# Performance work log

Measured on AMD Instinct MI355X. Metric: run time of the kernel, lower is better.

The kernel has to match this reference:

```python
import jax, jax.numpy as jnp
import numpy as np

MODEL_SIZE = 512
HEADS = 8
T = 2048
B = 2


def setup_inputs() -> dict:
    key = jax.random.key(0)
    ks = jax.random.split(key, 10)
    E = MODEL_SIZE
    w = 0.02  # weight init scale for numerical stability
    return {
        "input": jax.random.normal(ks[0], (T, B, E), jnp.float32),
        "pos": jax.random.normal(ks[1], (T, 1, E), jnp.float32),
        "in_proj_weight": jax.random.normal(ks[2], (3 * E, E), jnp.float32) * w,
        "out_proj_weight": jax.random.normal(ks[3], (E, E), jnp.float32) * w,
        "pos_proj_weight": jax.random.normal(ks[4], (E, E), jnp.float32) * w,
        "in_proj_bias": jax.random.normal(ks[5], (3 * E,), jnp.float32) * w,
        "out_proj_bias": jax.random.normal(ks[6], (E,), jnp.float32) * w,
        "pos_proj_bias": jax.random.normal(ks[7], (E,), jnp.float32) * w,
        "r_w_bias": jax.random.normal(ks[8], (HEADS, E // HEADS), jnp.float32) * w,
        "r_r_bias": jax.random.normal(ks[9], (HEADS, E // HEADS), jnp.float32) * w,
    }


def _rel_shift(x):
    # x: [B, H, T, R] -> Transformer-XL relative shift
    b, h, t, r = x.shape
    x = jnp.pad(x, ((0, 0), (0, 0), (0, 0), (1, 0)))  # [B,H,T,R+1]
    x = x.reshape(b, h, r + 1, t)[:, :, 1:, :]        # drop first row
    return x.reshape(b, h, t, r)


def reference(input, pos, in_proj_weight, out_proj_weight, pos_proj_weight,
              in_proj_bias, out_proj_bias, pos_proj_bias, r_w_bias, r_r_bias):
    t, b, e = input.shape
    h = r_w_bias.shape[0]
    d = e // h
    scale = 1.0 / np.sqrt(d).astype(np.float32)

    # fused QKV projection (time-first layout [T,B,E])
    qkv = input @ in_proj_weight.T + in_proj_bias          # [T,B,3E]
    q, k, v = jnp.split(qkv, 3, axis=-1)
    q = q.reshape(t, b, h, d)
    k = k.reshape(t, b, h, d)
    v = v.reshape(t, b, h, d)

    # relative position projection (pos batch dim is 1)
    r = (pos[:, 0] @ pos_proj_weight.T + pos_proj_bias).reshape(-1, h, d)  # [R,H,D]

    # content (AC) and position (BD) scores
    ac = jnp.einsum('tbhd,sbhd->bhts', q + r_w_bias, k)    # [B,H,T,T]
    bd = jnp.einsum('tbhd,rhd->bhtr', q + r_r_bias, r)     # [B,H,T,R]
    bd = _rel_shift(bd)[..., :t]

    attn = jax.nn.softmax((ac + bd) * scale, axis=-1)      # [B,H,T,T]
    ctx = jnp.einsum('bhts,sbhd->tbhd', attn, v).reshape(t, b, e)
    return ctx @ out_proj_weight.T + out_proj_bias
```

## Files before the change

kernel.cpp:

```cpp
#include <hip/hip_runtime.h>

#define T_SEQ 2048
#define BATCH 2
#define HEADS 8
#define DHEAD 64
#define EMB   512

typedef __attribute__((ext_vector_type(8))) short short8;
typedef __attribute__((ext_vector_type(4))) float floatx4;
typedef __attribute__((ext_vector_type(8))) unsigned short ushort8;
typedef __attribute__((ext_vector_type(4))) unsigned short ushort4v;

__device__ __forceinline__ unsigned short f2b(float f) {
    union { float f; unsigned u; } v; v.f = f;
    unsigned r = v.u + 0x7fffu + ((v.u >> 16) & 1u);
    return (unsigned short)(r >> 16);
}
__device__ __forceinline__ unsigned short f2bt(float f) {
    union { float f; unsigned u; } v; v.f = f;
    return (unsigned short)(v.u >> 16);
}
__device__ __forceinline__ float b2f(unsigned short s) {
    union { unsigned u; float f; } v; v.u = ((unsigned)s) << 16; return v.f;
}
__device__ __forceinline__ short8 ld_frag(const unsigned short* p) {
    ushort4v lo = *(const ushort4v*)p;
    ushort4v hi = *(const ushort4v*)(p + 4);
    short8 r;
    r[0] = lo[0]; r[1] = lo[1]; r[2] = lo[2]; r[3] = lo[3];
    r[4] = hi[0]; r[5] = hi[1]; r[6] = hi[2]; r[7] = hi[3];
    return r;
}
__device__ __forceinline__ void st8(unsigned short* p, ushort8 v) {
    ushort4v lo = { v[0], v[1], v[2], v[3] };
    ushort4v hi = { v[4], v[5], v[6], v[7] };
    *(ushort4v*)p = lo;
    *(ushort4v*)(p + 4) = hi;
}
__device__ __forceinline__ void gl16(const unsigned short* g, unsigned short* l) {
    __builtin_amdgcn_global_load_lds(
        (const __attribute__((address_space(1))) unsigned int*)g,
        (__attribute__((address_space(3))) unsigned int*)l, 16, 0, 0);
}
#define MFMA16(a, b, c) __builtin_amdgcn_mfma_f32_16x16x32_bf16(a, b, c, 0, 0, 0)

__global__ __launch_bounds__(256)
void cvt_all(const float* __restrict__ s0, const float* __restrict__ s1,
             const float* __restrict__ s2, const float* __restrict__ s3,
             const float* __restrict__ s4,
             unsigned short* __restrict__ d0, unsigned short* __restrict__ d1,
             unsigned short* __restrict__ d2, unsigned short* __restrict__ d3,
             unsigned short* __restrict__ d4)
{
    const int i = blockIdx.x * 256 + threadIdx.x;
    const float* s; unsigned short* d; int off;
    if      (i <  524288) { s = s0; d = d0; off = i; }
    else if (i <  786432) { s = s1; d = d1; off = i -  524288; }
    else if (i <  983040) { s = s2; d = d2; off = i -  786432; }
    else if (i < 1048576) { s = s3; d = d3; off = i -  983040; }
    else if (i < 1114112) { s = s4; d = d4; off = i - 1048576; }
    else return;
    const float4 v = ((const float4*)s)[off];
    ushort4v o = { f2b(v.x), f2b(v.y), f2b(v.z), f2b(v.w) };
    ((ushort4v*)d)[off] = o;
}

__global__ __launch_bounds__(256)
void gemm_qkv_pos(const unsigned short* __restrict__ inb, const unsigned short* __restrict__ w_inb,
                  const float* __restrict__ b_in,
                  const unsigned short* __restrict__ posb, const unsigned short* __restrict__ w_posb,
                  const float* __restrict__ b_pos,
                  unsigned short* __restrict__ q_s, unsigned short* __restrict__ k_s,
                  unsigned short* __restrict__ vT, unsigned short* __restrict__ r_b)
{
    __shared__ unsigned short shmem[24576];
    unsigned short* tb = shmem;

    const int id = blockIdx.x;
    const bool isPos = (id >= 768);
    const int bx = isPos ? ((id - 768) & 3) : (id % 12);
    const int by = isPos ? ((id - 768) >> 2) : (id / 12);
    const unsigned short* A = isPos ? posb : inb;
    const unsigned short* B = isPos ? w_posb : w_inb;
    const float* bias = isPos ? b_pos : b_in;

    const int bm  = by * 64;
    const int bn  = bx * 128;
    const int tid = threadIdx.x;
    const int lane = tid & 63, w = tid >> 6;
    const int m16 = lane & 15, quad = lane >> 4;
    const int wm = (w & 1) * 32, wn = (w >> 1) * 64;
    const int lrow = lane >> 3;
    const int lcol8 = lane & 7;

    floatx4 acc[2][4];
    #pragma unroll
    for (int i = 0; i < 2; ++i)
        #pragma unroll
        for (int j = 0; j < 4; ++j) acc[i][j] = (floatx4){0.f, 0.f, 0.f, 0.f};

    auto stage = [&](int q, int k0) {
        unsigned short* Ad = shmem + q * 12288;
        unsigned short* Bd = Ad + 4096;
        #pragma unroll
        for (int i = 0; i < 2; ++i) {
            const int rb  = w * 16 + i * 8;
            const int row = rb + lrow;
            const int sc  = ((lcol8 ^ (row & 7)) * 8);
            gl16(A + (size_t)(bm + row) * 512 + k0 + sc, Ad + rb * 64);
        }
        #pragma unroll
        for (int i = 0; i < 4; ++i) {
            const int rb  = w * 32 + i * 8;
            const int row = rb + lrow;
            const int sc  = ((lcol8 ^ (row & 7)) * 8);
            gl16(B + (size_t)(bn + row) * 512 + k0 + sc, Bd + rb * 64);
        }
    };
    auto frag = [&](const unsigned short* Ts, int row, int ks) {
        const int u = (ks * 4 + quad) ^ (row & 7);
        return ld_frag(&Ts[row * 64 + u * 8]);
    };

    stage(0, 0);
    __syncthreads();

    for (int kt = 0; kt < 8; ++kt) {
        const int p = kt & 1;
        unsigned short* As = shmem + p * 12288;
        unsigned short* Bs = As + 4096;
        if (kt + 1 < 8) stage(1 - p, (kt + 1) * 64);
        #pragma unroll
        for (int ks = 0; ks < 2; ++ks) {
            short8 af[2], bf[4];
            #pragma unroll
            for (int f = 0; f < 2; ++f)
                af[f] = frag(As, wm + f * 16 + m16, ks);
            #pragma unroll
            for (int f = 0; f < 4; ++f)
                bf[f] = frag(Bs, wn + f * 16 + m16, ks);
            #pragma unroll
            for (int fm = 0; fm < 2; ++fm)
                #pragma unroll
                for (int fn = 0; fn < 4; ++fn)
                    acc[fm][fn] = MFMA16(af[fm], bf[fn], acc[fm][fn]);
        }
        __syncthreads();
    }

    if (isPos) {
        #pragma unroll
        for (int fn = 0; fn < 4; ++fn) {
            const int n = bn + wn + fn * 16 + m16;
            const float bv = bias[n];
            #pragma unroll
            for (int fm = 0; fm < 2; ++fm)
                #pragma unroll
                for (int rgi = 0; rgi < 4; ++rgi) {
                    const int m = bm + wm + fm * 16 + quad * 4 + rgi;
                    r_b[(size_t)m * EMB + n] = f2b(acc[fm][fn][rgi] + bv);
                }
        }
    } else if (bn < 1024) {
        #pragma unroll
        for (int fn = 0; fn < 4; ++fn) {
            const int n = bn + wn + fn * 16 + m16;
            const float bv = bias[n];
            const int reg = n >> 9, c = n & 511, h = c >> 6, dd = c & 63;
            unsigned short* dst = reg == 0 ? q_s : k_s;
            #pragma unroll
            for (int fm = 0; fm < 2; ++fm)
                #pragma unroll
                for (int rgi = 0; rgi < 4; ++rgi) {
                    const int m = bm + wm + fm * 16 + quad * 4 + rgi;
                    const int t = m >> 1, b = m & 1;
                    dst[((size_t)(b * HEADS + h) * T_SEQ + t) * DHEAD + dd] = f2b(acc[fm][fn][rgi] + bv);
                }
        }
    } else {
        #pragma unroll
        for (int fn = 0; fn < 4; ++fn) {
            const int nl = wn + fn * 16 + m16;
            const float bv = bias[bn + nl];
            #pragma unroll
            for (int fm = 0; fm < 2; ++fm)
                #pragma unroll
                for (int rgi = 0; rgi < 4; ++rgi) {
                    const int ml = wm + fm * 16 + quad * 4 + rgi;
                    tb[nl * 67 + ml] = f2b(acc[fm][fn][rgi] + bv);
                }
        }
        __syncthreads();
        const int t0g = bm >> 1;
        for (int s2 = tid; s2 < 1024; s2 += 256) {
            const int nl = s2 >> 3;
            const int bsel = (s2 >> 2) & 1;
            const int j = s2 & 3;
            ushort8 o;
            #pragma unroll
            for (int k = 0; k < 8; ++k)
                o[k] = tb[nl * 67 + ((j * 8 + k) * 2 + bsel)];
            const int c = bn + nl - 1024, h = c >> 6, dd = c & 63;
            *(ushort8*)(vT + ((size_t)(bsel * HEADS + h) * DHEAD + dd) * T_SEQ + t0g + j * 8) = o;
        }
    }
}

__global__ __launch_bounds__(256)
void gemm_out(const unsigned short* __restrict__ A, const unsigned short* __restrict__ B,
              const float* __restrict__ bias, float* __restrict__ out)
{
    __shared__ unsigned short shmem[16384];
    const int bm  = blockIdx.y * 64;
    const int bn  = blockIdx.x * 64;
    const int tid = threadIdx.x;
    const int lane = tid & 63, w = tid >> 6;
    const int m16 = lane & 15, quad = lane >> 4;
    const int wm = (w & 1) * 32, wn = (w >> 1) * 32;
    const int lrow = lane >> 3;
    const int lcol8 = lane & 7;

    floatx4 acc[2][2];
    #pragma unroll
    for (int i = 0; i < 2; ++i)
        #pragma unroll
        for (int j = 0; j < 2; ++j) acc[i][j] = (floatx4){0.f, 0.f, 0.f, 0.f};

    auto stage = [&](int q, int k0) {
        unsigned short* Ad = shmem + q * 8192;
        unsigned short* Bd = Ad + 4096;
        #pragma unroll
        for (int i = 0; i < 2; ++i) {
            const int rb  = w * 16 + i * 8;
            const int row = rb + lrow;
            const int sc  = ((lcol8 ^ (row & 7)) * 8);
            gl16(A + (size_t)(bm + row) * 512 + k0 + sc, Ad + rb * 64);
            gl16(B + (size_t)(bn + row) * 512 + k0 + sc, Bd + rb * 64);
        }
    };
    auto frag = [&](const unsigned short* Ts, int row, int ks) {
        const int u = (ks * 4 + quad) ^ (row & 7);
        return ld_frag(&Ts[row * 64 + u * 8]);
    };

    stage(0, 0);
    __syncthreads();

    for (int kt = 0; kt < 8; ++kt) {
        const int p = kt & 1;
        unsigned short* As = shmem + p * 8192;
        unsigned short* Bs = As + 4096;
        if (kt + 1 < 8) stage(1 - p, (kt + 1) * 64);
        #pragma unroll
        for (int ks = 0; ks < 2; ++ks) {
            short8 af[2], bf[2];
            #pragma unroll
            for (int f = 0; f < 2; ++f) {
                af[f] = frag(As, wm + f * 16 + m16, ks);
                bf[f] = frag(Bs, wn + f * 16 + m16, ks);
            }
            #pragma unroll
            for (int fm = 0; fm < 2; ++fm)
                #pragma unroll
                for (int fn = 0; fn < 2; ++fn)
                    acc[fm][fn] = MFMA16(af[fm], bf[fn], acc[fm][fn]);
        }
        __syncthreads();
    }

    #pragma unroll
    for (int fn = 0; fn < 2; ++fn) {
        const int n = bn + wn + fn * 16 + m16;
        const float bv = bias[n];
        #pragma unroll
        for (int fm = 0; fm < 2; ++fm)
            #pragma unroll
            for (int rgi = 0; rgi < 4; ++rgi) {
                const int m = bm + wm + fm * 16 + quad * 4 + rgi;
                out[(size_t)m * EMB + n] = acc[fm][fn][rgi] + bv;
            }
    }
}

__global__ __launch_bounds__(256)
void attn_mfma(const unsigned short* __restrict__ qg_, const unsigned short* __restrict__ kg_,
               const unsigned short* __restrict__ vtg_, const unsigned short* __restrict__ rg_,
               const float* __restrict__ rwb, const float* __restrict__ rrb,
               unsigned short* __restrict__ ctx)
{
    const int T   = T_SEQ;
    const int tb  = blockIdx.x;
    const int t0  = tb * 64;
    const int bh  = blockIdx.y;
    const int h   = bh & 7;
    const int b   = bh >> 3;
    const int tid = threadIdx.x;
    const int lane = tid & 63;
    const int w    = tid >> 6;
    const int m16  = lane & 15;
    const int quad = lane >> 4;
    const int ibase = 16 * w + quad * 4;

    __shared__ unsigned short lds[38976];
    unsigned short* pbuf  = lds + 26112;
    unsigned short* ring  = lds + 30464;
    unsigned short* qrw_s = lds;
    unsigned short* qrr_s = lds + 8704;

    const unsigned short* qg  = qg_  + ((size_t)bh * T + t0) * DHEAD;
    const unsigned short* kg  = kg_  + (size_t)bh * T * DHEAD;
    const unsigned short* vtg = vtg_ + (size_t)bh * DHEAD * T;
    const unsigned short* rg  = rg_  + h * DHEAD;

    const float QSCALE = 0.125f * 1.44269504089f;
    for (int idx = tid; idx < 65 * 16; idx += 256) {
        const int row = idx >> 4, c = (idx & 15) << 2;
        ushort4v qv = {0, 0, 0, 0};
        if (t0 + row < T) qv = *(const ushort4v*)(qg + row * DHEAD + c);
        const float4 rr = *(const float4*)(rrb + h * DHEAD + c);
        qrr_s[row * 68 + c + 0] = f2b((b2f(qv[0]) + rr.x) * QSCALE);
        qrr_s[row * 68 + c + 1] = f2b((b2f(qv[1]) + rr.y) * QSCALE);
        qrr_s[row * 68 + c + 2] = f2b((b2f(qv[2]) + rr.z) * QSCALE);
        qrr_s[row * 68 + c + 3] = f2b((b2f(qv[3]) + rr.w) * QSCALE);
        if (row < 64) {
            const float4 rw = *(const float4*)(rwb + h * DHEAD + c);
            qrw_s[row * 68 + c + 0] = f2b((b2f(qv[0]) + rw.x) * QSCALE);
            qrw_s[row * 68 + c + 1] = f2b((b2f(qv[1]) + rw.y) * QSCALE);
            qrw_s[row * 68 + c + 2] = f2b((b2f(qv[2]) + rw.z) * QSCALE);
            qrw_s[row * 68 + c + 3] = f2b((b2f(qv[3]) + rw.w) * QSCALE);
        }
    }
    __syncthreads();

    short8 a_ac[2], a_qrl[2], a_qru[2];
    {
        const unsigned short* p0 = &qrw_s[(16 * w + m16) * 68 + quad * 8];
        a_ac[0]  = ld_frag(p0);  a_ac[1]  = ld_frag(p0 + 32);
        const unsigned short* p1 = &qrr_s[(16 * w + m16) * 68 + quad * 8];
        a_qrl[0] = ld_frag(p1);  a_qrl[1] = ld_frag(p1 + 32);
        const unsigned short* p2 = &qrr_s[(16 * w + 1 + m16) * 68 + quad * 8];
        a_qru[0] = ld_frag(p2);  a_qru[1] = ld_frag(p2 + 32);
    }

    const int srow0 = tid >> 3,          scol0 = (tid & 7) * 8;
    const int srow1 = (tid + 256) >> 3,  scol1 = (tid & 7) * 8;

    ushort8 kr[2], vr[2], rr8[2];
    auto prefetch = [&](int s0n) {
        const bool ln = (s0n <= t0);
        const int jb = (ln ? (s0n + T - t0 - 64) : (s0n - t0 - 65)) + 64;
        int j0 = jb + srow0; j0 = j0 < 0 ? 0 : (j0 > T - 1 ? T - 1 : j0);
        int j1 = jb + srow1; j1 = j1 < 0 ? 0 : (j1 > T - 1 ? T - 1 : j1);
        kr[0]  = *(const ushort8*)(kg + (size_t)(s0n + srow0) * DHEAD + scol0);
        kr[1]  = *(const ushort8*)(kg + (size_t)(s0n + srow1) * DHEAD + scol1);
        vr[0]  = *(const ushort8*)(vtg + (size_t)srow0 * T + s0n + scol0);
        vr[1]  = *(const ushort8*)(vtg + (size_t)srow1 * T + s0n + scol1);
        rr8[0] = *(const ushort8*)(rg + (size_t)j0 * EMB + scol0);
        rr8[1] = *(const ushort8*)(rg + (size_t)j1 * EMB + scol1);
    };
    auto store_bufs = [&](int q) {
        unsigned short* kb = lds + q * 4352;
        unsigned short* vb = lds + 8704 + q * 4352;
        unsigned short* rb = lds + 17408 + q * 4352;
        st8(&kb[srow0 * 68 + scol0], kr[0]);
        st8(&kb[srow1 * 68 + scol1], kr[1]);
        st8(&vb[srow0 * 68 + scol0], vr[0]);
        st8(&vb[srow1 * 68 + scol1], vr[1]);
        st8(&rb[srow0 * 68 + scol0], rr8[0]);
        st8(&rb[srow1 * 68 + scol1], rr8[1]);
    };
    auto stage_to = [&](unsigned short* dstb, int jbase) {
        #pragma unroll
        for (int idx = tid; idx < 512; idx += 256) {
            const int row = idx >> 3, c = (idx & 7) * 8;
            int j = jbase + row; j = j < 0 ? 0 : (j > T - 1 ? T - 1 : j);
            st8(&dstb[row * 68 + c], *(const ushort8*)(rg + (size_t)j * EMB + c));
        }
    };
    auto qr_half = [&](const unsigned short* rsb, const short8* aq, int slotbase) {
        #pragma unroll
        for (int cc = 0; cc < 4; ++cc) {
            floatx4 q4 = (floatx4){0.f, 0.f, 0.f, 0.f};
            #pragma unroll
            for (int ks = 0; ks < 2; ++ks) {
                short8 bfr = ld_frag(&rsb[(16 * cc + m16) * 68 + ks * 32 + quad * 8]);
                q4 = MFMA16(aq[ks], bfr, q4);
            }
            #pragma unroll
            for (int rgi = 0; rgi < 4; ++rgi)
                ring[(ibase + rgi) * 133 + slotbase + 16 * cc + m16] = f2bt(q4[rgi]);
        }
    };

    floatx4 O[4];
    float lrun[4];
    #pragma unroll
    for (int ct = 0; ct < 4; ++ct) O[ct] = (floatx4){0.f, 0.f, 0.f, 0.f};
    #pragma unroll
    for (int rgi = 0; rgi < 4; ++rgi) lrun[rgi] = 0.f;

    {
        stage_to(lds + 17408 + 4352, T - t0 - 64);
        prefetch(0);
        __syncthreads();
        qr_half(lds + 17408 + 4352, a_qrl, 0);
        store_bufs(0);
        __syncthreads();
    }

    for (int na = 0; na < T / 64; ++na) {
        const int s0 = na * 64;
        const int p = na & 1;
        unsigned short* kb = lds + p * 4352;
        unsigned short* vb = lds + 8704 + p * 4352;
        unsigned short* rp = lds + 17408 + p * 4352;
        const bool lower = (s0 <= t0);
        const int nph    = lower ? (s0 >> 6) : ((s0 - t0) >> 6);
        const int rbase  = (nph & 1) * 64;
        const int wbase  = 64 - rbase;
        const bool hasNext = (na + 1 < T / 64);

        floatx4 acf[4];
        __builtin_amdgcn_s_setprio(1);
        #pragma unroll
        for (int ct = 0; ct < 4; ++ct) {
            acf[ct] = (floatx4){0.f, 0.f, 0.f, 0.f};
            #pragma unroll
            for (int ks = 0; ks < 2; ++ks) {
                short8 bfr = ld_frag(&kb[(16 * ct + m16) * 68 + ks * 32 + quad * 8]);
                acf[ct] = MFMA16(a_ac[ks], bfr, acf[ct]);
            }
        }
        __builtin_amdgcn_s_setprio(0);
        if (hasNext) prefetch(s0 + 64);
        qr_half(rp, lower ? a_qrl : a_qru, wbase);

        if (s0 != t0) {
            #pragma unroll
            for (int ct = 0; ct < 4; ++ct) {
                #pragma unroll
                for (int rgi = 0; rgi < 4; ++rgi) {
                    const int i = ibase + rgi;
                    const int slot = ((63 - i + 16 * ct + m16) + rbase) & 127;
                    acf[ct][rgi] += b2f(ring[i * 133 + slot]);
                }
            }
            if (s0 == t0 + 64 && lane == 48 && w == 3)
                acf[0][3] -= b2f(ring[63 * 133 + (rbase & 127)]);
        } else {
            #pragma unroll
            for (int ct = 0; ct < 4; ++ct) {
                #pragma unroll
                for (int rgi = 0; rgi < 4; ++rgi) {
                    const int i = ibase + rgi, u = 16 * ct + m16;
                    if (u <= i) acf[ct][rgi] += b2f(ring[i * 133 + (((63 - i + u) + rbase) & 127)]);
                }
            }
            unsigned short* rpo = lds + 17408 + (1 - p) * 4352;
            __syncthreads();
            stage_to(rpo, -1);
            __syncthreads();
            qr_half(rpo, a_qru, 64);
            __syncthreads();
            #pragma unroll
            for (int ct = 0; ct < 4; ++ct) {
                #pragma unroll
                for (int rgi = 0; rgi < 4; ++rgi) {
                    const int i = ibase + rgi, u = 16 * ct + m16;
                    if (u >= i + 2) acf[ct][rgi] += b2f(ring[i * 133 + 63 - i + u]);
                }
            }
        }

        #pragma unroll
        for (int rgi = 0; rgi < 4; ++rgi) {
            #pragma unroll
            for (int ct = 0; ct < 4; ++ct) {
                const float pv = exp2f(acf[ct][rgi]);
                acf[ct][rgi] = pv;
                lrun[rgi] += pv;
            }
        }
        #pragma unroll
        for (int ct = 0; ct < 4; ++ct)
            #pragma unroll
            for (int rgi = 0; rgi < 4; ++rgi)
                pbuf[(ibase + rgi) * 68 + 16 * ct + m16] = f2bt(acf[ct][rgi]);

        short8 ap[2];
        {
            const unsigned short* pp = &pbuf[(16 * w + m16) * 68 + quad * 8];
            ap[0] = ld_frag(pp); ap[1] = ld_frag(pp + 32);
        }
        __builtin_amdgcn_s_setprio(1);
        #pragma unroll
        for (int ct = 0; ct < 4; ++ct) {
            #pragma unroll
            for (int ks = 0; ks < 2; ++ks) {
                short8 bfr = ld_frag(&vb[(16 * ct + m16) * 68 + ks * 32 + quad * 8]);
                O[ct] = MFMA16(ap[ks], bfr, O[ct]);
            }
        }
        __builtin_amdgcn_s_setprio(0);
        if (hasNext) store_bufs(1 - p);
        __syncthreads();
    }

    #pragma unroll
    for (int rgi = 0; rgi < 4; ++rgi) {
        float l = lrun[rgi];
        #pragma unroll
        for (int off = 1; off < 16; off <<= 1)
            l += __shfl_xor(l, off);
        const float inv = 1.f / l;
        const int t = t0 + ibase + rgi;
        #pragma unroll
        for (int ct = 0; ct < 4; ++ct)
            ctx[((size_t)t * BATCH + b) * EMB + h * DHEAD + 16 * ct + m16] = f2bt(O[ct][rgi] * inv);
    }
}

extern "C" void kernel_launch(void* const* d_in, const int* in_sizes, int n_in,
                              void* d_out, int out_size, void* d_ws, size_t ws_size,
                              hipStream_t stream)
{
    const float* input = (const float*)d_in[0];
    const float* pos   = (const float*)d_in[1];
    const float* w_in  = (const float*)d_in[2];
    const float* w_out = (const float*)d_in[3];
    const float* w_pos = (const float*)d_in[4];
    const float* b_in  = (const float*)d_in[5];
    const float* b_out = (const float*)d_in[6];
    const float* b_pos = (const float*)d_in[7];
    const float* rwb   = (const float*)d_in[8];
    const float* rrb   = (const float*)d_in[9];

    unsigned short* ws     = (unsigned short*)d_ws;
    unsigned short* inb    = ws;
    unsigned short* posb   = ws + 2097152;
    unsigned short* w_inb  = ws + 3145728;
    unsigned short* w_posb = ws + 3932160;
    unsigned short* w_outb = ws + 6291456;
    unsigned short* q_s    = ws + 6553600;
    unsigned short* k_s    = ws + 8650752;
    unsigned short* vT     = ws + 10747904;
    unsigned short* r_b    = ws + 12845056;
    unsigned short* ctx_b  = ws + 13893632;

    cvt_all<<<4352, 256, 0, stream>>>(input, pos, w_in, w_pos, w_out,
                                      inb, posb, w_inb, w_posb, w_outb);
    gemm_qkv_pos<<<896, 256, 0, stream>>>(inb, w_inb, b_in, posb, w_posb, b_pos,
                                          q_s, k_s, vT, r_b);
    attn_mfma<<<dim3(32, 16), 256, 0, stream>>>(q_s, k_s, vT, r_b, rwb, rrb, ctx_b);
    gemm_out<<<dim3(8, 64), 256, 0, stream>>>(ctx_b, w_outb, b_out, (float*)d_out);
}
```

Baseline: 183.2 us.

## Load relative-position R fragments directly from global into registers, bypassing LDS

The relative-position matrix R is no longer prefetched into a double-buffered LDS tile. Each wave now loads its MFMA B fragments for R straight from global memory into registers and feeds them to the Q·R MFMAs. This shrinks the shared-memory footprint, removes the extra staging and the three block-wide barriers on the diagonal tile, and should allow higher occupancy. The cost is per-wave global loads with less reuse and latency that is only partly hidden behind the AC MFMAs.

```diff
diff --git a/kernel.cpp b/kernel.cpp
--- a/kernel.cpp
+++ b/kernel.cpp
@@ -30,6 +30,11 @@
     r[0] = lo[0]; r[1] = lo[1]; r[2] = lo[2]; r[3] = lo[3];
     r[4] = hi[0]; r[5] = hi[1]; r[6] = hi[2]; r[7] = hi[3];
     return r;
+}
+__device__ __forceinline__ short8 ldg_frag(const unsigned short* p) {
+    union { ushort8 u; short8 s; } c;
+    c.u = *(const ushort8*)p;
+    return c.s;
 }
 __device__ __forceinline__ void st8(unsigned short* p, ushort8 v) {
     ushort4v lo = { v[0], v[1], v[2], v[3] };
@@ -301,11 +306,11 @@
     const int quad = lane >> 4;
     const int ibase = 16 * w + quad * 4;
 
-    __shared__ unsigned short lds[38976];
-    unsigned short* pbuf  = lds + 26112;
-    unsigned short* ring  = lds + 30464;
+    __shared__ unsigned short lds[30272];
+    unsigned short* pbuf  = lds + 17408;
+    unsigned short* ring  = lds + 21760;
     unsigned short* qrw_s = lds;
-    unsigned short* qrr_s = lds + 8704;
+    unsigned short* qrr_s = lds + 4352;
 
     const unsigned short* qg  = qg_  + ((size_t)bh * T + t0) * DHEAD;
     const unsigned short* kg  = kg_  + (size_t)bh * T * DHEAD;
@@ -345,47 +350,36 @@
     const int srow0 = tid >> 3,          scol0 = (tid & 7) * 8;
     const int srow1 = (tid + 256) >> 3,  scol1 = (tid & 7) * 8;
 
-    ushort8 kr[2], vr[2], rr8[2];
+    ushort8 kr[2], vr[2];
     auto prefetch = [&](int s0n) {
-        const bool ln = (s0n <= t0);
-        const int jb = (ln ? (s0n + T - t0 - 64) : (s0n - t0 - 65)) + 64;
-        int j0 = jb + srow0; j0 = j0 < 0 ? 0 : (j0 > T - 1 ? T - 1 : j0);
-        int j1 = jb + srow1; j1 = j1 < 0 ? 0 : (j1 > T - 1 ? T - 1 : j1);
         kr[0]  = *(const ushort8*)(kg + (size_t)(s0n + srow0) * DHEAD + scol0);
         kr[1]  = *(const ushort8*)(kg + (size_t)(s0n + srow1) * DHEAD + scol1);
         vr[0]  = *(const ushort8*)(vtg + (size_t)srow0 * T + s0n + scol0);
         vr[1]  = *(const ushort8*)(vtg + (size_t)srow1 * T + s0n + scol1);
-        rr8[0] = *(const ushort8*)(rg + (size_t)j0 * EMB + scol0);
-        rr8[1] = *(const ushort8*)(rg + (size_t)j1 * EMB + scol1);
     };
     auto store_bufs = [&](int q) {
         unsigned short* kb = lds + q * 4352;
         unsigned short* vb = lds + 8704 + q * 4352;
-        unsigned short* rb = lds + 17408 + q * 4352;
         st8(&kb[srow0 * 68 + scol0], kr[0]);
         st8(&kb[srow1 * 68 + scol1], kr[1]);
         st8(&vb[srow0 * 68 + scol0], vr[0]);
         st8(&vb[srow1 * 68 + scol1], vr[1]);
-        st8(&rb[srow0 * 68 + scol0], rr8[0]);
-        st8(&rb[srow1 * 68 + scol1], rr8[1]);
-    };
-    auto stage_to = [&](unsigned short* dstb, int jbase) {
-        #pragma unroll
-        for (int idx = tid; idx < 512; idx += 256) {
-            const int row = idx >> 3, c = (idx & 7) * 8;
-            int j = jbase + row; j = j < 0 ? 0 : (j > T - 1 ? T - 1 : j);
-            st8(&dstb[row * 68 + c], *(const ushort8*)(rg + (size_t)j * EMB + c));
-        }
-    };
-    auto qr_half = [&](const unsigned short* rsb, const short8* aq, int slotbase) {
+    };
+    auto ldR = [&](int jbase, short8 (&rr)[4][2]) {
+        #pragma unroll
+        for (int cc = 0; cc < 4; ++cc) {
+            int j = jbase + 16 * cc + m16; j = j < 0 ? 0 : (j > T - 1 ? T - 1 : j);
+            const unsigned short* rrow = rg + (size_t)j * EMB + quad * 8;
+            rr[cc][0] = ldg_frag(rrow);
+            rr[cc][1] = ldg_frag(rrow + 32);
+        }
+    };
+    auto qr_from = [&](short8 (&rr)[4][2], const short8* aq, int slotbase) {
         #pragma unroll
         for (int cc = 0; cc < 4; ++cc) {
             floatx4 q4 = (floatx4){0.f, 0.f, 0.f, 0.f};
-            #pragma unroll
-            for (int ks = 0; ks < 2; ++ks) {
-                short8 bfr = ld_frag(&rsb[(16 * cc + m16) * 68 + ks * 32 + quad * 8]);
-                q4 = MFMA16(aq[ks], bfr, q4);
-            }
+            q4 = MFMA16(aq[0], rr[cc][0], q4);
+            q4 = MFMA16(aq[1], rr[cc][1], q4);
             #pragma unroll
             for (int rgi = 0; rgi < 4; ++rgi)
                 ring[(ibase + rgi) * 133 + slotbase + 16 * cc + m16] = f2bt(q4[rgi]);
@@ -399,11 +393,12 @@
     #pragma unroll
     for (int rgi = 0; rgi < 4; ++rgi) lrun[rgi] = 0.f;
 
+    short8 rf[4][2];
     {
-        stage_to(lds + 17408 + 4352, T - t0 - 64);
+        ldR(T - t0 - 64, rf);
         prefetch(0);
         __syncthreads();
-        qr_half(lds + 17408 + 4352, a_qrl, 0);
+        qr_from(rf, a_qrl, 0);
         store_bufs(0);
         __syncthreads();
     }
@@ -413,12 +408,14 @@
         const int p = na & 1;
         unsigned short* kb = lds + p * 4352;
         unsigned short* vb = lds + 8704 + p * 4352;
-        unsigned short* rp = lds + 17408 + p * 4352;
         const bool lower = (s0 <= t0);
         const int nph    = lower ? (s0 >> 6) : ((s0 - t0) >> 6);
         const int rbase  = (nph & 1) * 64;
         const int wbase  = 64 - rbase;
+        const bool diag  = (s0 == t0);
         const bool hasNext = (na + 1 < T / 64);
+
+        if (!diag) ldR(lower ? (s0 + T - t0) : (s0 - t0 - 1), rf);
 
         floatx4 acf[4];
         __builtin_amdgcn_s_setprio(1);
@@ -433,9 +430,9 @@
         }
         __builtin_amdgcn_s_setprio(0);
         if (hasNext) prefetch(s0 + 64);
-        qr_half(rp, lower ? a_qrl : a_qru, wbase);
-
-        if (s0 != t0) {
+
+        if (!diag) {
+            qr_from(rf, lower ? a_qrl : a_qru, wbase);
             #pragma unroll
             for (int ct = 0; ct < 4; ++ct) {
                 #pragma unroll
@@ -456,12 +453,8 @@
                     if (u <= i) acf[ct][rgi] += b2f(ring[i * 133 + (((63 - i + u) + rbase) & 127)]);
                 }
             }
-            unsigned short* rpo = lds + 17408 + (1 - p) * 4352;
-            __syncthreads();
-            stage_to(rpo, -1);
-            __syncthreads();
-            qr_half(rpo, a_qru, 64);
-            __syncthreads();
+            ldR(-1, rf);
+            qr_from(rf, a_qru, 64);
             #pragma unroll
             for (int ct = 0; ct < 4; ++ct) {
                 #pragma unroll
```

New measurement: 213.0 us. 1.16x slower.
